# Kernel tuning notes

Hardware: AMD Instinct MI355X
Metric: run time of the kernel (lower is better)

## Reference

```python
import jax, jax.numpy as jnp
import numpy as np

N = 50000      # nodes
E = 800000     # edges per graph (avg degree 16)
F_IN = 256     # input feature dim
H = 64         # hidden dim
K = 32         # number of pure sources / topics
NEG_SLOPE = 0.2


def _add_self_loops(ei, n):
    loop = jnp.arange(n, dtype=ei.dtype)
    return jnp.concatenate([ei, jnp.stack([loop, loop])], axis=1)


def _gatv2(x, ei, Wl, Wr, att, bias, n):
    """PyG GATv2Conv, heads=1: e_ij = att . leaky_relu(Wl x_j + Wr x_i),
    softmax over incoming edges per target i, out_i = sum_j alpha_ij * Wl x_j + bias."""
    src, dst = ei[0], ei[1]            # edge j -> i  (source, target)
    xl = x @ Wl                        # [n, H] source transform (also the message)
    xr = x @ Wr                        # [n, H] target transform
    msg = xl[src]                      # [E, H] gathered source messages
    s = jax.nn.leaky_relu(msg + xr[dst], negative_slope=NEG_SLOPE) @ att  # [E]
    # numerically stable segment softmax over dst
    smax = jax.ops.segment_max(s, dst, num_segments=n)
    ex = jnp.exp(s - smax[dst])
    denom = jax.ops.segment_sum(ex, dst, num_segments=n)
    alpha = ex / (denom[dst] + 1e-16)
    out = jax.ops.segment_sum(msg * alpha[:, None], dst, num_segments=n)
    return out + bias


def setup_inputs() -> dict:
    key = jax.random.key(0)
    ks = jax.random.split(key, 14)
    X = jax.random.normal(ks[0], (N, F_IN), jnp.float32)
    ei_feat = jax.random.randint(ks[1], (2, E), 0, N, dtype=jnp.int64)
    ei_spatial = jax.random.randint(ks[2], (2, E), 0, N, dtype=jnp.int64)
    s1 = 1.0 / np.sqrt(F_IN)
    s2 = 1.0 / np.sqrt(H)
    Wl1 = jax.random.normal(ks[3], (F_IN, H), jnp.float32) * s1
    Wr1 = jax.random.normal(ks[4], (F_IN, H), jnp.float32) * s1
    att1 = jax.random.normal(ks[5], (H,), jnp.float32) * s2
    b1 = jnp.zeros((H,), jnp.float32)
    Wl2 = jax.random.normal(ks[6], (H, K), jnp.float32) * s2
    Wr2 = jax.random.normal(ks[7], (H, K), jnp.float32) * s2
    att2 = jax.random.normal(ks[8], (K,), jnp.float32) * (1.0 / np.sqrt(K))
    b2 = jnp.zeros((K,), jnp.float32)
    M = jax.random.uniform(ks[9], (K, F_IN), jnp.float32)
    edge_w = jax.random.normal(ks[10], (1,), jnp.float32)
    return {"X": X, "ei_feat": ei_feat, "ei_spatial": ei_spatial,
            "Wl1": Wl1, "Wr1": Wr1, "att1": att1, "b1": b1,
            "Wl2": Wl2, "Wr2": Wr2, "att2": att2, "b2": b2,
            "M": M, "edge_w": edge_w}


def reference(X, ei_feat, ei_spatial, Wl1, Wr1, att1, b1, Wl2, Wr2, att2, b2, M, edge_w):
    ei = _add_self_loops(ei_feat, N)
    h = jax.nn.elu(_gatv2(X, ei, Wl1, Wr1, att1, b1, N))          # [N, H]
    Z = jax.nn.softmax(_gatv2(h, ei, Wl2, Wr2, att2, b2, N), axis=1)  # [N, K]
    X_pure = Z @ jax.nn.relu(M)                                   # [N, F]
    row, col = ei_spatial[0], ei_spatial[1]
    w = jax.nn.sigmoid(edge_w)                                    # (1,)
    contam = jax.ops.segment_sum(X_pure[col], row, num_segments=N)  # scatter_add
    return Z, X_pure + w * contam, w
```

## Files before the change

### kernel.cpp

```cpp
#include <hip/hip_runtime.h>
#include <math.h>

#define N_NODES 50000
#define E_EDGES 800000
#define F_INDIM 256
#define H_DIM   64
#define K_DIM   32
#define NEG_SLOPE 0.2f

#define SLOT 64
#define RANGE_N 12500
#define FILL_WGPG 128
#define FILL_SLICE (E_EDGES / FILL_WGPG)
#define NFILL_BLK 1024
#define NGEMM_BLK 782
#define FB 16

typedef short short8v __attribute__((ext_vector_type(8)));
typedef unsigned short us8 __attribute__((ext_vector_type(8)));
typedef float f32x4 __attribute__((ext_vector_type(4)));

__device__ __forceinline__ unsigned short f2bf(float f) {
    unsigned u = __float_as_uint(f);
    unsigned r = (u + 0x7FFFu + ((u >> 16) & 1u)) >> 16;
    return (unsigned short)r;
}
__device__ __forceinline__ float bf2f(unsigned short h) {
    return __uint_as_float(((unsigned)h) << 16);
}

template<int CTRL>
__device__ __forceinline__ float dpp_xadd(float v) {
    int x = __builtin_amdgcn_update_dpp(0, __float_as_int(v), CTRL, 0xF, 0xF, true);
    return v + __int_as_float(x);
}
template<int CTRL>
__device__ __forceinline__ float dpp_xmax(float v) {
    int x = __builtin_amdgcn_update_dpp(0, __float_as_int(v), CTRL, 0xF, 0xF, true);
    return fmaxf(v, __int_as_float(x));
}
__device__ __forceinline__ float red_sum64(float v) {
    v = dpp_xadd<0xB1>(v); v = dpp_xadd<0x4E>(v);
    v = dpp_xadd<0x141>(v); v = dpp_xadd<0x140>(v);
    v += __shfl_xor(v, 16, 64);
    v += __shfl_xor(v, 32, 64);
    return v;
}
__device__ __forceinline__ float red_sum32(float v) {
    v = dpp_xadd<0xB1>(v); v = dpp_xadd<0x4E>(v);
    v = dpp_xadd<0x141>(v); v = dpp_xadd<0x140>(v);
    v += __shfl_xor(v, 16, 64);
    return v;
}
__device__ __forceinline__ float red_max32(float v) {
    v = dpp_xmax<0xB1>(v); v = dpp_xmax<0x4E>(v);
    v = dpp_xmax<0x141>(v); v = dpp_xmax<0x140>(v);
    v = fmaxf(v, __shfl_xor(v, 16, 64));
    return v;
}

__global__ __launch_bounds__(256) void prep_kernel(
        const float* __restrict__ Wl, const float* __restrict__ Wr,
        unsigned short* __restrict__ Bh, unsigned short* __restrict__ Bl,
        int* __restrict__ curF, int* __restrict__ curS) {
    const int t = blockIdx.x * 256 + threadIdx.x;
    if (t < N_NODES) { curF[t] = t * SLOT; curS[t] = t * SLOT; }
    if (t >= 4096) return;
    const int lane = t & 63;
    const int ks = (t >> 6) & 7;
    const int ct = t >> 9;
    const int n = ct * 16 + (lane & 15);
    const int kbase = ks * 32 + (lane >> 4) * 8;
    const float* W = (n < H_DIM) ? Wl : Wr;
    const int col = n & 63;
#pragma unroll
    for (int e = 0; e < 8; ++e) {
        float w = W[(size_t)(kbase + e) * H_DIM + col];
        unsigned short hi = f2bf(w);
        unsigned short lo = f2bf(w - bf2f(hi));
        Bh[(size_t)t * 8 + e] = hi;
        Bl[(size_t)t * 8 + e] = lo;
    }
}

__global__ __launch_bounds__(256) void gemmfill_kernel(
        const float* __restrict__ X,
        const unsigned short* __restrict__ Bh, const unsigned short* __restrict__ Bl,
        unsigned short* __restrict__ xlb, float* __restrict__ xr,
        const int* __restrict__ srcF, const int* __restrict__ dstF,
        const int* __restrict__ colS, const int* __restrict__ rowS,
        int* __restrict__ curF, int* __restrict__ curS,
        int* __restrict__ csrF, int* __restrict__ csrS) {
    if (blockIdx.x < NFILL_BLK) {
        const int wg = blockIdx.x;
        const int g  = wg & 7;
        const int j  = wg >> 3;
        const int e0 = j * FILL_SLICE, e1 = e0 + FILL_SLICE;
        const bool feat = (g < 4);
        const int base = (feat ? g : g - 4) * RANGE_N;
        const int* dA = feat ? dstF : rowS;
        const int* sA = feat ? srcF : colS;
        int* cur = feat ? curF : curS;
        int* csr = feat ? csrF : csrS;

        for (int eb = e0 + (int)threadIdx.x; eb < e1; eb += 256 * FB) {
            int d[FB], s[FB];
            bool ok[FB];
#pragma unroll
            for (int k = 0; k < FB; ++k) {
                const int e = eb + k * 256;
                const bool inr = (e < e1);
                const int ee = inr ? e : e0;
                d[k] = __builtin_nontemporal_load(&dA[ee]);
                s[k] = __builtin_nontemporal_load(&sA[ee]);
                ok[k] = inr && ((unsigned)(d[k] - base) < RANGE_N);
            }
            int p[FB];
#pragma unroll
            for (int k = 0; k < FB; ++k)
                if (ok[k]) p[k] = atomicAdd(&cur[d[k]], 1);
#pragma unroll
            for (int k = 0; k < FB; ++k)
                if (ok[k] && p[k] < (d[k] + 1) * SLOT) csr[p[k]] = s[k];
        }
    } else {
        const int blk = blockIdx.x - NFILL_BLK;
        const int wv = threadIdx.x >> 6;
        const int lane = threadIdx.x & 63;
        const int m0 = blk * 64 + wv * 16;
        const int r = lane & 15;
        const int g = lane >> 4;
        int arow = m0 + r;
        if (arow > N_NODES - 1) arow = N_NODES - 1;
        const float* xrow = X + (size_t)arow * F_INDIM + g * 8;

        f32x4 acc[8];
#pragma unroll
        for (int c = 0; c < 8; ++c) acc[c] = (f32x4){0.f, 0.f, 0.f, 0.f};

        for (int ks = 0; ks < 8; ++ks) {
            const float4 f0 = *(const float4*)(xrow + ks * 32);
            const float4 f1 = *(const float4*)(xrow + ks * 32 + 4);
            float f[8] = {f0.x, f0.y, f0.z, f0.w, f1.x, f1.y, f1.z, f1.w};
            union { us8 u; short8v s; } Ah, Al;
#pragma unroll
            for (int j = 0; j < 8; ++j) {
                unsigned short hi = f2bf(f[j]);
                Ah.u[j] = hi;
                Al.u[j] = f2bf(f[j] - bf2f(hi));
            }
            union { us8 u; short8v s; } bh[8], bl[8];
#pragma unroll
            for (int ct = 0; ct < 8; ++ct) {
                const size_t fo = ((size_t)(ct * 8 + ks) * 64 + lane) * 8;
                bh[ct].u = *(const us8*)(Bh + fo);
                bl[ct].u = *(const us8*)(Bl + fo);
            }
#pragma unroll
            for (int ct = 0; ct < 8; ++ct)
                acc[ct] = __builtin_amdgcn_mfma_f32_16x16x32_bf16(Ah.s, bh[ct].s, acc[ct], 0, 0, 0);
#pragma unroll
            for (int ct = 0; ct < 8; ++ct)
                acc[ct] = __builtin_amdgcn_mfma_f32_16x16x32_bf16(Ah.s, bl[ct].s, acc[ct], 0, 0, 0);
#pragma unroll
            for (int ct = 0; ct < 8; ++ct)
                acc[ct] = __builtin_amdgcn_mfma_f32_16x16x32_bf16(Al.s, bh[ct].s, acc[ct], 0, 0, 0);
        }
#pragma unroll
        for (int ct = 0; ct < 8; ++ct) {
            const int n = ct * 16 + r;
            const int col = n & 63;
#pragma unroll
            for (int i = 0; i < 4; ++i) {
                const int rr = m0 + g * 4 + i;
                if (rr < N_NODES) {
                    if (n < H_DIM) xlb[(size_t)rr * H_DIM + col] = f2bf(acc[ct][i]);
                    else           xr[(size_t)rr * H_DIM + col] = acc[ct][i];
                }
            }
        }
    }
}

__global__ __launch_bounds__(256) void agg1_kernel(
        const int* __restrict__ curF, const int* __restrict__ csrF,
        const unsigned short* __restrict__ xlb, const float* __restrict__ xr,
        const float* __restrict__ att1, const float* __restrict__ b1,
        const float* __restrict__ Wl2, const float* __restrict__ Wr2,
        unsigned short* __restrict__ xl2b, float* __restrict__ xr2) {
    __shared__ float hs[4][H_DIM];
    const int wid  = threadIdx.x >> 6;
    const int lane = threadIdx.x & 63;
    const int n = blockIdx.x * 4 + wid;
    const float xrv  = xr[(size_t)n * H_DIM + lane];
    const float attv = att1[lane];
    const int start = n * SLOT;
    const int cnt = min(__builtin_amdgcn_readfirstlane(curF[n]) - start, SLOT) + 1;
    float m = -1e30f, den = 0.f, acc = 0.f;
    int srcs[8];
#pragma unroll
    for (int j = 0; j < 8; ++j) srcs[j] = (j < cnt - 1) ? csrF[start + j] : n;
    for (int t0 = 0; t0 < cnt; t0 += 8) {
        float xc[8];
#pragma unroll
        for (int j = 0; j < 8; ++j) xc[j] = bf2f(xlb[(size_t)srcs[j] * H_DIM + lane]);
        int nsrcs[8];
#pragma unroll
        for (int j = 0; j < 8; ++j) {
            int t = t0 + 8 + j;
            nsrcs[j] = (t < cnt - 1) ? csrF[start + t] : n;
        }
        float v[8];
#pragma unroll
        for (int j = 0; j < 8; ++j) {
            float a = xc[j] + xrv;
            a = a > 0.f ? a : NEG_SLOPE * a;
            v[j] = a * attv;
        }
#pragma unroll
        for (int j = 0; j < 8; ++j) v[j] = red_sum64(v[j]);
        float vmax = -1e30f;
#pragma unroll
        for (int j = 0; j < 8; ++j) {
            if (t0 + j >= cnt) v[j] = -1e30f;
            vmax = fmaxf(vmax, v[j]);
        }
        const float mn = fmaxf(m, vmax);
        const float sc = __expf(m - mn);
        acc *= sc; den *= sc;
#pragma unroll
        for (int j = 0; j < 8; ++j) {
            const float p = __expf(v[j] - mn);
            acc += p * xc[j];
            den += p;
        }
        m = mn;
#pragma unroll
        for (int j = 0; j < 8; ++j) srcs[j] = nsrcs[j];
    }
    float h = acc / den + b1[lane];
    h = h > 0.f ? h : expm1f(h);
    hs[wid][lane] = h;
    __syncthreads();
    const float* W = (lane < K_DIM) ? Wl2 : Wr2;
    const int col = lane & 31;
    float s = 0.f;
#pragma unroll
    for (int k = 0; k < H_DIM; ++k) s += hs[wid][k] * W[k * K_DIM + col];
    if (lane < K_DIM) xl2b[(size_t)n * K_DIM + col] = f2bf(s);
    else              xr2[(size_t)n * K_DIM + col] = s;
}

__global__ __launch_bounds__(256) void agg2_kernel(
        const int* __restrict__ curF, const int* __restrict__ csrF,
        const unsigned short* __restrict__ xl2b, const float* __restrict__ xr2,
        const float* __restrict__ att2, const float* __restrict__ b2,
        float* __restrict__ Z, unsigned short* __restrict__ Zb) {
    const int t = blockIdx.x * 256 + threadIdx.x;
    const int n = t >> 5;
    const int sub = t & 31;
    if (n >= N_NODES) return;
    const float xrv  = xr2[(size_t)n * K_DIM + sub];
    const float attv = att2[sub];
    const int start = n * SLOT;
    const int cnt = min(curF[n] - start, SLOT) + 1;
    float m = -1e30f, den = 0.f, acc = 0.f;
    int srcs[8];
#pragma unroll
    for (int j = 0; j < 8; ++j) srcs[j] = (j < cnt - 1) ? csrF[start + j] : n;
    for (int t0 = 0; t0 < cnt; t0 += 8) {
        float xc[8];
#pragma unroll
        for (int j = 0; j < 8; ++j) xc[j] = bf2f(xl2b[(size_t)srcs[j] * K_DIM + sub]);
        int nsrcs[8];
#pragma unroll
        for (int j = 0; j < 8; ++j) {
            int tt = t0 + 8 + j;
            nsrcs[j] = (tt < cnt - 1) ? csrF[start + tt] : n;
        }
        float v[8];
#pragma unroll
        for (int j = 0; j < 8; ++j) {
            float a = xc[j] + xrv;
            a = a > 0.f ? a : NEG_SLOPE * a;
            v[j] = a * attv;
        }
#pragma unroll
        for (int j = 0; j < 8; ++j) v[j] = red_sum32(v[j]);
        float vmax = -1e30f;
#pragma unroll
        for (int j = 0; j < 8; ++j) {
            if (t0 + j >= cnt) v[j] = -1e30f;
            vmax = fmaxf(vmax, v[j]);
        }
        const float mn = fmaxf(m, vmax);
        const float sc = __expf(m - mn);
        acc *= sc; den *= sc;
#pragma unroll
        for (int j = 0; j < 8; ++j) {
            const float p = __expf(v[j] - mn);
            acc += p * xc[j];
            den += p;
        }
        m = mn;
#pragma unroll
        for (int j = 0; j < 8; ++j) srcs[j] = nsrcs[j];
    }
    float z = acc / den + b2[sub];
    float mx = red_max32(z);
    float e = __expf(z - mx);
    float ssum = red_sum32(e);
    const float zv = e / ssum;
    Z[(size_t)n * K_DIM + sub] = zv;
    Zb[(size_t)n * K_DIM + sub] = f2bf(zv);
}

__global__ __launch_bounds__(256) void saggfinal_kernel(
        const int* __restrict__ curS, const int* __restrict__ csrS,
        const unsigned short* __restrict__ Zb, const float* __restrict__ Z,
        const float* __restrict__ M, const float* __restrict__ edge_w,
        float* __restrict__ out2, float* __restrict__ wout) {
    __shared__ float zs[8][K_DIM];
    const int n0 = blockIdx.x * 8;
    const int tid = threadIdx.x;
    const float w = 1.f / (1.f + __expf(-edge_w[0]));
    {
        const int hw = tid >> 5;
        const int sub = tid & 31;
        const int n = n0 + hw;
        const int start = n * SLOT;
        const int endi = start + min(curS[n] - start, SLOT);
        float acc = 0.f;
        for (int t0 = start; t0 < endi; t0 += 8) {
            float val[8];
#pragma unroll
            for (int j = 0; j < 8; ++j) {
                int tt = t0 + j;
                int c = csrS[tt < endi ? tt : (endi - 1)];
                val[j] = bf2f(Zb[(size_t)c * K_DIM + sub]);
            }
#pragma unroll
            for (int j = 0; j < 8; ++j)
                acc += (t0 + j < endi) ? val[j] : 0.f;
        }
        zs[hw][sub] = Z[(size_t)n * K_DIM + sub] + w * acc;
    }
    __syncthreads();
    float Mr[K_DIM];
#pragma unroll
    for (int k = 0; k < K_DIM; ++k) Mr[k] = fmaxf(M[k * F_INDIM + tid], 0.f);
#pragma unroll
    for (int q = 0; q < 8; ++q) {
        float acc = 0.f;
#pragma unroll
        for (int k = 0; k < K_DIM; ++k) acc += zs[q][k] * Mr[k];
        out2[(size_t)(n0 + q) * F_INDIM + tid] = acc;
    }
    if (n0 == 0 && tid == 0) wout[0] = w;
}

extern "C" void kernel_launch(void* const* d_in, const int* in_sizes, int n_in,
                              void* d_out, int out_size, void* d_ws, size_t ws_size,
                              hipStream_t stream) {
    const float* X    = (const float*)d_in[0];
    const int*   eif  = (const int*)d_in[1];
    const int*   eis  = (const int*)d_in[2];
    const float* Wl1  = (const float*)d_in[3];
    const float* Wr1  = (const float*)d_in[4];
    const float* att1 = (const float*)d_in[5];
    const float* b1   = (const float*)d_in[6];
    const float* Wl2  = (const float*)d_in[7];
    const float* Wr2  = (const float*)d_in[8];
    const float* att2 = (const float*)d_in[9];
    const float* b2   = (const float*)d_in[10];
    const float* M    = (const float*)d_in[11];
    const float* ew   = (const float*)d_in[12];

    const int* srcF = eif;
    const int* dstF = eif + E_EDGES;
    const int* rowS = eis;
    const int* colS = eis + E_EDGES;

    const size_t N = N_NODES;
    char* ws = (char*)d_ws;
    size_t off = 0;
    auto alloc = [&](size_t bytes) { char* p = ws + off; off += (bytes + 255) & ~(size_t)255; return p; };

    unsigned short* xlb = (unsigned short*)alloc(N * H_DIM * sizeof(unsigned short));
    float* xr1  = (float*)alloc(N * H_DIM * sizeof(float));
    unsigned short* xl2b = (unsigned short*)alloc(N * K_DIM * sizeof(unsigned short));
    float* xr2  = (float*)alloc(N * K_DIM * sizeof(float));
    unsigned short* Zb = (unsigned short*)alloc(N * K_DIM * sizeof(unsigned short));
    int*   curF = (int*)alloc(N * sizeof(int));
    int*   curS = (int*)alloc(N * sizeof(int));
    int*   csrF = (int*)alloc((size_t)N * SLOT * sizeof(int));
    int*   csrS = (int*)alloc((size_t)N * SLOT * sizeof(int));
    unsigned short* Bh = (unsigned short*)alloc(4096 * 8 * sizeof(unsigned short));
    unsigned short* Bl = (unsigned short*)alloc(4096 * 8 * sizeof(unsigned short));

    float* Z    = (float*)d_out;
    float* out2 = (float*)d_out + N * (size_t)K_DIM;
    float* wout = (float*)d_out + N * (size_t)(K_DIM + F_INDIM);

    prep_kernel<<<(N_NODES + 255) / 256, 256, 0, stream>>>(Wl1, Wr1, Bh, Bl, curF, curS);
    gemmfill_kernel<<<NFILL_BLK + NGEMM_BLK, 256, 0, stream>>>(
        X, Bh, Bl, xlb, xr1, srcF, dstF, colS, rowS, curF, curS, csrF, csrS);

    agg1_kernel<<<N_NODES / 4, 256, 0, stream>>>(curF, csrF, xlb, xr1, att1, b1,
                                                 Wl2, Wr2, xl2b, xr2);
    agg2_kernel<<<(N_NODES * K_DIM + 255) / 256, 256, 0, stream>>>(curF, csrF,
                                                                   xl2b, xr2, att2, b2,
                                                                   Z, Zb);
    saggfinal_kernel<<<N_NODES / 8, 256, 0, stream>>>(curS, csrS, Zb, Z, M, ew, out2, wout);
}
```

Before: 220.1 us.

## Move spatial CSR fill into agg1 launch to overlap with aggregation

The spatial-graph CSR fill moves out of the GEMM+feature-fill kernel and into the first aggregation kernel as extra leading blocks, so it overlaps with agg1 instead of with the GEMM. Each fill now covers one graph with 8 destination ranges of 6250 nodes, and the per-thread batch drops from 16 to 8 edges. This rebalances work across launches and shortens the first fused kernel. The risk is that the atomics-heavy fill blocks compete with agg1's gathers.

Result: slower. 231.7 us (+5.3%).

```diff
diff --git a/kernel.cpp b/kernel.cpp
--- a/kernel.cpp
+++ b/kernel.cpp
@@ -9,12 +9,13 @@
 #define NEG_SLOPE 0.2f
 
 #define SLOT 64
-#define RANGE_N 12500
+#define RANGE_N 6250
 #define FILL_WGPG 128
 #define FILL_SLICE (E_EDGES / FILL_WGPG)
 #define NFILL_BLK 1024
 #define NGEMM_BLK 782
-#define FB 16
+#define NAGG1_BLK 12500
+#define FB 8
 
 typedef short short8v __attribute__((ext_vector_type(8)));
 typedef unsigned short us8 __attribute__((ext_vector_type(8)));
@@ -57,6 +58,35 @@
     v = dpp_xmax<0x141>(v); v = dpp_xmax<0x140>(v);
     v = fmaxf(v, __shfl_xor(v, 16, 64));
     return v;
+}
+
+__device__ __forceinline__ void fill_body(
+        const int* __restrict__ dA, const int* __restrict__ sA,
+        int* __restrict__ cur, int* __restrict__ csr, int wg) {
+    const int g  = wg & 7;
+    const int j  = wg >> 3;
+    const int e0 = j * FILL_SLICE, e1 = e0 + FILL_SLICE;
+    const int base = g * RANGE_N;
+    for (int eb = e0 + (int)threadIdx.x; eb < e1; eb += 256 * FB) {
+        int d[FB], s[FB];
+        bool ok[FB];
+#pragma unroll
+        for (int k = 0; k < FB; ++k) {
+            const int e = eb + k * 256;
+            const bool inr = (e < e1);
+            const int ee = inr ? e : e0;
+            d[k] = __builtin_nontemporal_load(&dA[ee]);
+            s[k] = __builtin_nontemporal_load(&sA[ee]);
+            ok[k] = inr && ((unsigned)(d[k] - base) < RANGE_N);
+        }
+        int p[FB];
+#pragma unroll
+        for (int k = 0; k < FB; ++k)
+            if (ok[k]) p[k] = atomicAdd(&cur[d[k]], 1);
+#pragma unroll
+        for (int k = 0; k < FB; ++k)
+            if (ok[k] && p[k] < (d[k] + 1) * SLOT) csr[p[k]] = s[k];
+    }
 }
 
 __global__ __launch_bounds__(256) void prep_kernel(
@@ -83,46 +113,14 @@
     }
 }
 
-__global__ __launch_bounds__(256) void gemmfill_kernel(
+__global__ __launch_bounds__(256) void gemmfillF_kernel(
         const float* __restrict__ X,
         const unsigned short* __restrict__ Bh, const unsigned short* __restrict__ Bl,
         unsigned short* __restrict__ xlb, float* __restrict__ xr,
         const int* __restrict__ srcF, const int* __restrict__ dstF,
-        const int* __restrict__ colS, const int* __restrict__ rowS,
-        int* __restrict__ curF, int* __restrict__ curS,
-        int* __restrict__ csrF, int* __restrict__ csrS) {
+        int* __restrict__ curF, int* __restrict__ csrF) {
     if (blockIdx.x < NFILL_BLK) {
-        const int wg = blockIdx.x;
-        const int g  = wg & 7;
-        const int j  = wg >> 3;
-        const int e0 = j * FILL_SLICE, e1 = e0 + FILL_SLICE;
-        const bool feat = (g < 4);
-        const int base = (feat ? g : g - 4) * RANGE_N;
-        const int* dA = feat ? dstF : rowS;
-        const int* sA = feat ? srcF : colS;
-        int* cur = feat ? curF : curS;
-        int* csr = feat ? csrF : csrS;
-
-        for (int eb = e0 + (int)threadIdx.x; eb < e1; eb += 256 * FB) {
-            int d[FB], s[FB];
-            bool ok[FB];
-#pragma unroll
-            for (int k = 0; k < FB; ++k) {
-                const int e = eb + k * 256;
-                const bool inr = (e < e1);
-                const int ee = inr ? e : e0;
-                d[k] = __builtin_nontemporal_load(&dA[ee]);
-                s[k] = __builtin_nontemporal_load(&sA[ee]);
-                ok[k] = inr && ((unsigned)(d[k] - base) < RANGE_N);
-            }
-            int p[FB];
-#pragma unroll
-            for (int k = 0; k < FB; ++k)
-                if (ok[k]) p[k] = atomicAdd(&cur[d[k]], 1);
-#pragma unroll
-            for (int k = 0; k < FB; ++k)
-                if (ok[k] && p[k] < (d[k] + 1) * SLOT) csr[p[k]] = s[k];
-        }
+        fill_body(dstF, srcF, curF, csrF, blockIdx.x);
     } else {
         const int blk = blockIdx.x - NFILL_BLK;
         const int wv = threadIdx.x >> 6;
@@ -182,16 +180,23 @@
     }
 }
 
-__global__ __launch_bounds__(256) void agg1_kernel(
+__global__ __launch_bounds__(256) void agg1fillS_kernel(
+        const int* __restrict__ colS, const int* __restrict__ rowS,
+        int* __restrict__ curS, int* __restrict__ csrS,
         const int* __restrict__ curF, const int* __restrict__ csrF,
         const unsigned short* __restrict__ xlb, const float* __restrict__ xr,
         const float* __restrict__ att1, const float* __restrict__ b1,
         const float* __restrict__ Wl2, const float* __restrict__ Wr2,
         unsigned short* __restrict__ xl2b, float* __restrict__ xr2) {
+    if (blockIdx.x < NFILL_BLK) {
+        fill_body(rowS, colS, curS, csrS, blockIdx.x);
+        return;
+    }
     __shared__ float hs[4][H_DIM];
+    const int blk = blockIdx.x - NFILL_BLK;
     const int wid  = threadIdx.x >> 6;
     const int lane = threadIdx.x & 63;
-    const int n = blockIdx.x * 4 + wid;
+    const int n = blk * 4 + wid;
     const float xrv  = xr[(size_t)n * H_DIM + lane];
     const float attv = att1[lane];
     const int start = n * SLOT;
@@ -403,11 +408,11 @@
     float* wout = (float*)d_out + N * (size_t)(K_DIM + F_INDIM);
 
     prep_kernel<<<(N_NODES + 255) / 256, 256, 0, stream>>>(Wl1, Wr1, Bh, Bl, curF, curS);
-    gemmfill_kernel<<<NFILL_BLK + NGEMM_BLK, 256, 0, stream>>>(
-        X, Bh, Bl, xlb, xr1, srcF, dstF, colS, rowS, curF, curS, csrF, csrS);
-
-    agg1_kernel<<<N_NODES / 4, 256, 0, stream>>>(curF, csrF, xlb, xr1, att1, b1,
-                                                 Wl2, Wr2, xl2b, xr2);
+    gemmfillF_kernel<<<NFILL_BLK + NGEMM_BLK, 256, 0, stream>>>(
+        X, Bh, Bl, xlb, xr1, srcF, dstF, curF, csrF);
+    agg1fillS_kernel<<<NFILL_BLK + NAGG1_BLK, 256, 0, stream>>>(
+        colS, rowS, curS, csrS, curF, csrF, xlb, xr1, att1, b1,
+        Wl2, Wr2, xl2b, xr2);
     agg2_kernel<<<(N_NODES * K_DIM + 255) / 256, 256, 0, stream>>>(curF, csrF,
                                                                    xl2b, xr2, att2, b2,
                                                                    Z, Zb);
```
